# Performance work log

Hardware: AMD Instinct MI355X
Metric: run time of the kernel (lower is better)

The kernel has to match this reference:

```python
import jax, jax.numpy as jnp
import numpy as np

C = 19          # EEG channels
NP = C * C      # 361 channel pairs
D = 256         # UNIFIED_FEATURE_DIM
H = 8           # num_heads
HD = D // H     # head dim


def _build_mask():
    # rel[p, q] = True iff key-pair q shares a channel with query-pair p
    idx = np.arange(NP)
    ci, cj = idx // C, idx % C
    rel = ((ci[:, None] == ci[None, :]) | (ci[:, None] == cj[None, :]) |
           (cj[:, None] == ci[None, :]) | (cj[:, None] == cj[None, :]))
    return jnp.asarray(rel.reshape(C, C, NP))  # (channel_i, j, key_pair)

MASK = _build_mask()


def setup_inputs() -> dict:
    key = jax.random.key(0)
    ks = jax.random.split(key, 6)
    s = 0.05
    return {
        "x": jax.random.normal(ks[0], (32, NP, D), jnp.float32),
        # 19 stacked nn.MultiheadAttention modules: in_proj (3D, D) = [Wq; Wk; Wv]
        "w_in": jax.random.normal(ks[1], (C, 3 * D, D), jnp.float32) * s,
        "b_in": jnp.zeros((C, 3 * D), jnp.float32),
        "w_out": jax.random.normal(ks[2], (C, D, D), jnp.float32) * s,
        "b_out": jnp.zeros((C, D), jnp.float32),
        # fusion: nn.Linear(D, D)
        "w_fuse": jax.random.normal(ks[3], (D, D), jnp.float32) * s,
        "b_fuse": jnp.zeros((D,), jnp.float32),
    }


def reference(x, w_in, b_in, w_out, b_out, w_fuse, b_fuse):
    # x: (B, 361, D). Pair p=(i,j) at index i*19+j uses attention module i,
    # query = x[:, p], keys/values = pairs sharing channel i or j (mask).
    B = x.shape[0]
    wq, wk, wv = w_in[:, :D], w_in[:, D:2 * D], w_in[:, 2 * D:]
    bq, bk, bv = b_in[:, :D], b_in[:, D:2 * D], b_in[:, 2 * D:]

    # Per-channel K/V projections over all 361 pairs: (C, B, NP, D)
    K = jnp.einsum('bnd,ced->cbne', x, wk) + bk[:, None, None, :]
    V = jnp.einsum('bnd,ced->cbne', x, wv) + bv[:, None, None, :]
    # Queries grouped by first channel i: x reshaped to (B, C, C, D)
    xq = x.reshape(B, C, C, D)
    Q = jnp.einsum('bcjd,ced->cbje', xq, wq) + bq[:, None, None, :]  # (C,B,C,D)

    Qh = Q.reshape(C, B, C, H, HD)
    Kh = K.reshape(C, B, NP, H, HD)
    Vh = V.reshape(C, B, NP, H, HD)

    scale = 1.0 / jnp.sqrt(jnp.asarray(HD, x.dtype))
    scores = jnp.einsum('cbqhe,cbkhe->cbhqk', Qh, Kh) * scale  # (C,B,H,C,NP)
    scores = jnp.where(MASK[:, None, None, :, :], scores, -jnp.inf)
    attn = jax.nn.softmax(scores, axis=-1)

    out = jnp.einsum('cbhqk,cbkhe->cbqhe', attn, Vh).reshape(C, B, C, D)
    out = jnp.einsum('cbqd,ced->cbqe', out, w_out) + b_out[:, None, None, :]
    out = out.transpose(1, 0, 2, 3).reshape(B, NP, D)  # back to (B, 361, D)

    # fusion ('linear') + residual
    return out @ w_fuse.T + b_fuse + x
```

## Files before the change

### kernel.cpp

```cpp
#include <hip/hip_runtime.h>

#define CC 19
#define NPOS 361
#define NPAD 384
#define DIM 256
#define TKEY 32
#define NTILES 12

#define LDS_BYTES 33792

using bf16x8 = __attribute__((ext_vector_type(8))) short;
using f16x4  = __attribute__((ext_vector_type(4))) _Float16;
using floatx4 = __attribute__((ext_vector_type(4))) float;
using uintx2 = __attribute__((ext_vector_type(2))) unsigned int;

__device__ __forceinline__ unsigned short f2bf(float f) {
  unsigned u = __builtin_bit_cast(unsigned, f);
  u += 0x7fffu + ((u >> 16) & 1u);
  return (unsigned short)(u >> 16);
}

__device__ __forceinline__ f16x4 pack4h(float a, float b, float c2, float d) {
  const auto h01 = __builtin_amdgcn_cvt_pkrtz(a, b);
  const auto h23 = __builtin_amdgcn_cvt_pkrtz(c2, d);
  uintx2 uv = {__builtin_bit_cast(unsigned, h01), __builtin_bit_cast(unsigned, h23)};
  return __builtin_bit_cast(f16x4, uv);
}

__global__ void conv_all_kernel(const float* __restrict__ x,
                                const float* __restrict__ w_in,
                                const float* __restrict__ w_out,
                                const float* __restrict__ w_fuse,
                                unsigned short* __restrict__ ws) {
  const int j = blockIdx.x * 256 + threadIdx.x;
  float4 v = make_float4(0.f, 0.f, 0.f, 0.f);
  unsigned short* dst;
  if (j < 786432) {
    const int row = j >> 6;
    const int off = (j & 63) << 2;
    const int b = row / NPAD;
    const int r = row - b * NPAD;
    if (r < NPOS) v = *(const float4*)&x[(b * NPOS + r) * DIM + off];
    dst = &ws[row * DIM + off];
  } else if (j < 1720320) {
    const int k = j - 786432;
    v = *(const float4*)&w_in[k << 2];
    dst = &ws[3145728 + (k << 2)];
  } else if (j < 2031616) {
    const int k = j - 1720320;
    v = *(const float4*)&w_out[k << 2];
    dst = &ws[6881280 + (k << 2)];
  } else {
    const int k = j - 2031616;
    v = *(const float4*)&w_fuse[k << 2];
    dst = &ws[8126464 + (k << 2)];
  }
  ushort4 o;
  o.x = f2bf(v.x); o.y = f2bf(v.y); o.z = f2bf(v.z); o.w = f2bf(v.w);
  *(ushort4*)dst = o;
}

__launch_bounds__(512, 2)
__global__ void cgca_kernel(const float* __restrict__ xf,
                            const float* __restrict__ b_in,
                            const float* __restrict__ b_out,
                            const float* __restrict__ b_fuse,
                            const unsigned short* __restrict__ xbf,
                            const unsigned short* __restrict__ wibf,
                            const unsigned short* __restrict__ wobf,
                            const unsigned short* __restrict__ wfbf,
                            float* __restrict__ out) {
  const int bid = blockIdx.x;
  const int xcd = bid & 7;
  const int slot = bid >> 3;
  int c, b;
  if (slot < 64) {
    c = ((slot >> 5) << 3) + xcd;
    b = slot & 31;
  } else {
    const int widx = ((slot - 64) << 3) + xcd;
    c = 16 + (widx >> 5);
    b = widx & 31;
  }

  const int tid = threadIdx.x;
  const int w = tid >> 6;
  const int lane = tid & 63;
  const int quad = lane >> 4;
  const int l16 = lane & 15;
  const int eh = w * 32;

  extern __shared__ char smem[];
  unsigned short* bufx0 = (unsigned short*)(smem);
  unsigned short* bufx1 = (unsigned short*)(smem + 16896);
  float* sL = (float*)(smem + 16896);

  const float scale = 0.17677669529663687f;
  const floatx4 fzero = {0.f, 0.f, 0.f, 0.f};

  f16x4 qf[2][2];
  {
    bf16x8 wq[2][8];
#pragma unroll
    for (int m4 = 0; m4 < 2; ++m4)
#pragma unroll
      for (int k = 0; k < 8; ++k)
        wq[m4][k] = *(const bf16x8*)&wibf[(c * 768 + eh + m4 * 16 + l16) * DIM + k * 32 + quad * 8];
    float bq[2][4];
#pragma unroll
    for (int m4 = 0; m4 < 2; ++m4) {
      const float4 bv4 = *(const float4*)&b_in[c * 768 + eh + m4 * 16 + quad * 4];
      bq[m4][0] = bv4.x; bq[m4][1] = bv4.y; bq[m4][2] = bv4.z; bq[m4][3] = bv4.w;
    }
#pragma unroll
    for (int mt = 0; mt < 2; ++mt) {
      const int xrow = b * NPAD + c * CC + mt * 16 + l16;
      bf16x8 xq[8];
#pragma unroll
      for (int k = 0; k < 8; ++k)
        xq[k] = *(const bf16x8*)&xbf[xrow * DIM + k * 32 + quad * 8];
#pragma unroll
      for (int m4 = 0; m4 < 2; ++m4) {
        floatx4 acc = fzero;
#pragma unroll
        for (int k = 0; k < 8; ++k)
          acc = __builtin_amdgcn_mfma_f32_16x16x32_bf16(wq[m4][k], xq[k], acc, 0, 0, 0);
        qf[mt][m4] = pack4h((acc[0] + bq[m4][0]) * scale, (acc[1] + bq[m4][1]) * scale,
                            (acc[2] + bq[m4][2]) * scale, (acc[3] + bq[m4][3]) * scale);
      }
    }
  }

  bf16x8 wk[2][8], wv[2][8];
#pragma unroll
  for (int m4 = 0; m4 < 2; ++m4)
#pragma unroll
    for (int k = 0; k < 8; ++k) {
      wk[m4][k] =
          *(const bf16x8*)&wibf[(c * 768 + 256 + eh + m4 * 16 + l16) * DIM + k * 32 + quad * 8];
      wv[m4][k] =
          *(const bf16x8*)&wibf[(c * 768 + 512 + eh + m4 * 16 + l16) * DIM + k * 32 + quad * 8];
    }
  float bk[2][4];
#pragma unroll
  for (int m4 = 0; m4 < 2; ++m4) {
    const float4 bv4 = *(const float4*)&b_in[c * 768 + 256 + eh + m4 * 16 + quad * 4];
    bk[m4][0] = bv4.x; bk[m4][1] = bv4.y; bk[m4][2] = bv4.z; bk[m4][3] = bv4.w;
  }
  float bV[2];
#pragma unroll
  for (int ne = 0; ne < 2; ++ne) bV[ne] = b_in[c * 768 + 512 + eh + ne * 16 + l16];

#pragma unroll
  for (int it = 0; it < 2; ++it) {
    const int cc2 = tid + it * 512;
    const int row = cc2 >> 5;
    const int col = (cc2 & 31) * 8;
    *(bf16x8*)&bufx0[row * 264 + col] = *(const bf16x8*)&xbf[(b * NPAD + row) * DIM + col];
  }

  floatx4 o_acc[2][2];
  float lsum[2] = {0.f, 0.f};
#pragma unroll
  for (int mt = 0; mt < 2; ++mt)
#pragma unroll
    for (int ne = 0; ne < 2; ++ne) o_acc[mt][ne] = fzero;

  __syncthreads();

  for (int t = 0; t < NTILES; ++t) {
    const int t0 = t * TKEY;
    unsigned short* bx  = (t & 1) ? bufx1 : bufx0;
    unsigned short* bxn = (t & 1) ? bufx0 : bufx1;

    if (t + 1 < NTILES) {
#pragma unroll
      for (int it = 0; it < 2; ++it) {
        const int cc2 = tid + it * 512;
        const int row = cc2 >> 5;
        const int col = (cc2 & 31) * 8;
        *(bf16x8*)&bxn[row * 264 + col] =
            *(const bf16x8*)&xbf[(b * NPAD + t0 + TKEY + row) * DIM + col];
      }
    }

    floatx4 aK[2][2], aV[2][2];
#pragma unroll
    for (int i = 0; i < 2; ++i)
#pragma unroll
      for (int j = 0; j < 2; ++j) { aK[i][j] = fzero; aV[i][j] = fzero; }
#pragma unroll
    for (int k = 0; k < 8; ++k) {
      bf16x8 xfr[2];
#pragma unroll
      for (int n4 = 0; n4 < 2; ++n4)
        xfr[n4] = *(const bf16x8*)&bx[(n4 * 16 + l16) * 264 + k * 32 + quad * 8];
#pragma unroll
      for (int m4 = 0; m4 < 2; ++m4)
#pragma unroll
        for (int n4 = 0; n4 < 2; ++n4) {
          aK[m4][n4] = __builtin_amdgcn_mfma_f32_16x16x32_bf16(wk[m4][k], xfr[n4], aK[m4][n4], 0, 0, 0);
          aV[n4][m4] = __builtin_amdgcn_mfma_f32_16x16x32_bf16(xfr[n4], wv[m4][k], aV[n4][m4], 0, 0, 0);
        }
    }
    __syncthreads();

    f16x4 kf[2][2];
    f16x4 vf[2][2];
#pragma unroll
    for (int kt = 0; kt < 2; ++kt)
#pragma unroll
      for (int ec = 0; ec < 2; ++ec) {
        kf[kt][ec] = pack4h(aK[ec][kt][0] + bk[ec][0], aK[ec][kt][1] + bk[ec][1],
                            aK[ec][kt][2] + bk[ec][2], aK[ec][kt][3] + bk[ec][3]);
        vf[kt][ec] = pack4h(aV[kt][ec][0] + bV[ec], aV[kt][ec][1] + bV[ec],
                            aV[kt][ec][2] + bV[ec], aV[kt][ec][3] + bV[ec]);
      }

#pragma unroll
    for (int mt = 0; mt < 2; ++mt) {
      const unsigned q = (unsigned)(mt * 16 + l16);
      f16x4 pf[2];
#pragma unroll
      for (int kt = 0; kt < 2; ++kt) {
        floatx4 s = __builtin_amdgcn_mfma_f32_16x16x16f16(kf[kt][0], qf[mt][0], fzero, 0, 0, 0);
        s = __builtin_amdgcn_mfma_f32_16x16x16f16(kf[kt][1], qf[mt][1], s, 0, 0, 0);
        const int kbase = t0 + kt * 16 + quad * 4;
        float p[4];
#pragma unroll
        for (int r = 0; r < 4; ++r) {
          const int kabs = kbase + r;
          const unsigned ki = ((unsigned)kabs * 110377u) >> 21;
          const unsigned kj = (unsigned)kabs - ki * 19u;
          const bool ok = (kabs < NPOS) &&
                          (ki == (unsigned)c || kj == (unsigned)c || ki == q || kj == q);
          p[r] = ok ? __expf(s[r]) : 0.f;
        }
        lsum[mt] += (p[0] + p[1]) + (p[2] + p[3]);
        pf[kt] = pack4h(p[0], p[1], p[2], p[3]);
      }
#pragma unroll
      for (int kt = 0; kt < 2; ++kt)
#pragma unroll
        for (int ne = 0; ne < 2; ++ne)
          o_acc[mt][ne] =
              __builtin_amdgcn_mfma_f32_16x16x16f16(pf[kt], vf[kt][ne], o_acc[mt][ne], 0, 0, 0);
    }
  }

#pragma unroll
  for (int mt = 0; mt < 2; ++mt) {
    lsum[mt] += __shfl_xor(lsum[mt], 16);
    lsum[mt] += __shfl_xor(lsum[mt], 32);
  }
  if (lane < 16) {
    sL[w * 32 + lane] = lsum[0];
    sL[w * 32 + 16 + lane] = lsum[1];
  }
  float invl[2][4];
#pragma unroll
  for (int mt = 0; mt < 2; ++mt)
#pragma unroll
    for (int r = 0; r < 4; ++r)
      invl[mt][r] = 1.f / sL[w * 32 + mt * 16 + quad * 4 + r];

#pragma unroll
  for (int mt = 0; mt < 2; ++mt)
#pragma unroll
    for (int ne = 0; ne < 2; ++ne)
#pragma unroll
      for (int r = 0; r < 4; ++r)
        bufx0[(mt * 16 + quad * 4 + r) * 264 + eh + ne * 16 + l16] =
            f2bf(o_acc[mt][ne][r] * invl[mt][r]);
  __syncthreads();

#pragma unroll
  for (int mt = 0; mt < 2; ++mt) {
    bf16x8 a8[8];
#pragma unroll
    for (int k = 0; k < 8; ++k)
      a8[k] = *(const bf16x8*)&bufx0[(mt * 16 + l16) * 264 + k * 32 + quad * 8];
#pragma unroll
    for (int nt2 = 0; nt2 < 2; ++nt2) {
      const int e0 = w * 32 + nt2 * 16;
      floatx4 acc = fzero;
#pragma unroll
      for (int k = 0; k < 8; ++k) {
        bf16x8 b8 = *(const bf16x8*)&wobf[(c * 256 + e0 + l16) * DIM + k * 32 + quad * 8];
        acc = __builtin_amdgcn_mfma_f32_16x16x32_bf16(a8[k], b8, acc, 0, 0, 0);
      }
      const float bias = b_out[c * 256 + e0 + l16];
#pragma unroll
      for (int r = 0; r < 4; ++r)
        bufx1[(mt * 16 + quad * 4 + r) * 264 + e0 + l16] = f2bf(acc[r] + bias);
    }
  }
  __syncthreads();

#pragma unroll
  for (int mt = 0; mt < 2; ++mt) {
    bf16x8 a8[8];
#pragma unroll
    for (int k = 0; k < 8; ++k)
      a8[k] = *(const bf16x8*)&bufx1[(mt * 16 + l16) * 264 + k * 32 + quad * 8];
#pragma unroll
    for (int nt2 = 0; nt2 < 2; ++nt2) {
      const int e0 = w * 32 + nt2 * 16;
      floatx4 acc = fzero;
#pragma unroll
      for (int k = 0; k < 8; ++k) {
        bf16x8 b8 = *(const bf16x8*)&wfbf[(e0 + l16) * DIM + k * 32 + quad * 8];
        acc = __builtin_amdgcn_mfma_f32_16x16x32_bf16(a8[k], b8, acc, 0, 0, 0);
      }
      const float bfu = b_fuse[e0 + l16];
#pragma unroll
      for (int r = 0; r < 4; ++r) {
        const int row = mt * 16 + quad * 4 + r;
        if (row < CC) {
          const int gp = (b * NPOS + c * CC + row) * DIM + e0 + l16;
          out[gp] = acc[r] + bfu + xf[gp];
        }
      }
    }
  }
}

extern "C" void kernel_launch(void* const* d_in, const int* in_sizes, int n_in,
                              void* d_out, int out_size, void* d_ws, size_t ws_size,
                              hipStream_t stream) {
  const float* x      = (const float*)d_in[0];
  const float* w_in   = (const float*)d_in[1];
  const float* b_in   = (const float*)d_in[2];
  const float* w_out  = (const float*)d_in[3];
  const float* b_out  = (const float*)d_in[4];
  const float* w_fuse = (const float*)d_in[5];
  const float* b_fuse = (const float*)d_in[6];
  float* out = (float*)d_out;

  if (ws_size < (size_t)16384000) return;

  unsigned short* ws = (unsigned short*)d_ws;
  unsigned short* x_bf  = ws;
  unsigned short* wi_bf = ws + 3145728;
  unsigned short* wo_bf = ws + 6881280;
  unsigned short* wf_bf = ws + 8126464;

  conv_all_kernel<<<8000, 256, 0, stream>>>(x, w_in, w_out, w_fuse, ws);

  (void)hipFuncSetAttribute((const void*)cgca_kernel,
                            hipFuncAttributeMaxDynamicSharedMemorySize, LDS_BYTES);
  cgca_kernel<<<608, 512, LDS_BYTES, stream>>>(x, b_in, b_out, b_fuse, x_bf, wi_bf,
                                               wo_bf, wf_bf, out);
}
```

Baseline: 253.6 us.

## Stream Wk/Wv weights from global per tile instead of holding in registers

Stops keeping the K and V projection weight fragments resident in registers across all key tiles. Each tile now reloads them from global/L2 inside the loop and computes K and V in separate scoped blocks, which cuts register pressure. Launch bounds go from 2 to 4 waves-per-SIMD to raise occupancy. The cost is repeated weight loads every tile (12x more weight traffic through the cache), and there is a risk of memory stalls or spills under the tighter register budget.

```diff
diff --git a/kernel.cpp b/kernel.cpp
--- a/kernel.cpp
+++ b/kernel.cpp
@@ -60,7 +60,7 @@
   *(ushort4*)dst = o;
 }
 
-__launch_bounds__(512, 2)
+__launch_bounds__(512, 4)
 __global__ void cgca_kernel(const float* __restrict__ xf,
                             const float* __restrict__ b_in,
                             const float* __restrict__ b_out,
@@ -98,58 +98,37 @@
   const float scale = 0.17677669529663687f;
   const floatx4 fzero = {0.f, 0.f, 0.f, 0.f};
 
+  float bq[2][4], bk[2][4], bV[2];
+#pragma unroll
+  for (int m4 = 0; m4 < 2; ++m4) {
+    const float4 q4 = *(const float4*)&b_in[c * 768 + eh + m4 * 16 + quad * 4];
+    bq[m4][0] = q4.x; bq[m4][1] = q4.y; bq[m4][2] = q4.z; bq[m4][3] = q4.w;
+    const float4 k4 = *(const float4*)&b_in[c * 768 + 256 + eh + m4 * 16 + quad * 4];
+    bk[m4][0] = k4.x; bk[m4][1] = k4.y; bk[m4][2] = k4.z; bk[m4][3] = k4.w;
+    bV[m4] = b_in[c * 768 + 512 + eh + m4 * 16 + l16];
+  }
+
   f16x4 qf[2][2];
-  {
-    bf16x8 wq[2][8];
-#pragma unroll
-    for (int m4 = 0; m4 < 2; ++m4)
-#pragma unroll
-      for (int k = 0; k < 8; ++k)
-        wq[m4][k] = *(const bf16x8*)&wibf[(c * 768 + eh + m4 * 16 + l16) * DIM + k * 32 + quad * 8];
-    float bq[2][4];
+#pragma unroll
+  for (int mt = 0; mt < 2; ++mt) {
+    const int xrow = b * NPAD + c * CC + mt * 16 + l16;
+    bf16x8 xq[8];
+#pragma unroll
+    for (int k = 0; k < 8; ++k)
+      xq[k] = *(const bf16x8*)&xbf[xrow * DIM + k * 32 + quad * 8];
 #pragma unroll
     for (int m4 = 0; m4 < 2; ++m4) {
-      const float4 bv4 = *(const float4*)&b_in[c * 768 + eh + m4 * 16 + quad * 4];
-      bq[m4][0] = bv4.x; bq[m4][1] = bv4.y; bq[m4][2] = bv4.z; bq[m4][3] = bv4.w;
-    }
-#pragma unroll
-    for (int mt = 0; mt < 2; ++mt) {
-      const int xrow = b * NPAD + c * CC + mt * 16 + l16;
-      bf16x8 xq[8];
-#pragma unroll
-      for (int k = 0; k < 8; ++k)
-        xq[k] = *(const bf16x8*)&xbf[xrow * DIM + k * 32 + quad * 8];
-#pragma unroll
-      for (int m4 = 0; m4 < 2; ++m4) {
-        floatx4 acc = fzero;
-#pragma unroll
-        for (int k = 0; k < 8; ++k)
-          acc = __builtin_amdgcn_mfma_f32_16x16x32_bf16(wq[m4][k], xq[k], acc, 0, 0, 0);
-        qf[mt][m4] = pack4h((acc[0] + bq[m4][0]) * scale, (acc[1] + bq[m4][1]) * scale,
-                            (acc[2] + bq[m4][2]) * scale, (acc[3] + bq[m4][3]) * scale);
-      }
-    }
-  }
-
-  bf16x8 wk[2][8], wv[2][8];
-#pragma unroll
-  for (int m4 = 0; m4 < 2; ++m4)
-#pragma unroll
-    for (int k = 0; k < 8; ++k) {
-      wk[m4][k] =
-          *(const bf16x8*)&wibf[(c * 768 + 256 + eh + m4 * 16 + l16) * DIM + k * 32 + quad * 8];
-      wv[m4][k] =
-          *(const bf16x8*)&wibf[(c * 768 + 512 + eh + m4 * 16 + l16) * DIM + k * 32 + quad * 8];
-    }
-  float bk[2][4];
-#pragma unroll
-  for (int m4 = 0; m4 < 2; ++m4) {
-    const float4 bv4 = *(const float4*)&b_in[c * 768 + 256 + eh + m4 * 16 + quad * 4];
-    bk[m4][0] = bv4.x; bk[m4][1] = bv4.y; bk[m4][2] = bv4.z; bk[m4][3] = bv4.w;
-  }
-  float bV[2];
-#pragma unroll
-  for (int ne = 0; ne < 2; ++ne) bV[ne] = b_in[c * 768 + 512 + eh + ne * 16 + l16];
+      const unsigned short* wqp = &wibf[(c * 768 + eh + m4 * 16 + l16) * DIM + quad * 8];
+      floatx4 acc = fzero;
+#pragma unroll
+      for (int k = 0; k < 8; ++k) {
+        const bf16x8 wq = *(const bf16x8*)(wqp + k * 32);
+        acc = __builtin_amdgcn_mfma_f32_16x16x32_bf16(wq, xq[k], acc, 0, 0, 0);
+      }
+      qf[mt][m4] = pack4h((acc[0] + bq[m4][0]) * scale, (acc[1] + bq[m4][1]) * scale,
+                          (acc[2] + bq[m4][2]) * scale, (acc[3] + bq[m4][3]) * scale);
+    }
+  }
 
 #pragma unroll
   for (int it = 0; it < 2; ++it) {
@@ -165,6 +144,9 @@
   for (int mt = 0; mt < 2; ++mt)
 #pragma unroll
     for (int ne = 0; ne < 2; ++ne) o_acc[mt][ne] = fzero;
+
+  const unsigned short* wkbase = &wibf[(c * 768 + 256 + eh + l16) * DIM + quad * 8];
+  const unsigned short* wvbase = &wibf[(c * 768 + 512 + eh + l16) * DIM + quad * 8];
 
   __syncthreads();
 
@@ -184,38 +166,66 @@
       }
     }
 
-    floatx4 aK[2][2], aV[2][2];
-#pragma unroll
-    for (int i = 0; i < 2; ++i)
-#pragma unroll
-      for (int j = 0; j < 2; ++j) { aK[i][j] = fzero; aV[i][j] = fzero; }
-#pragma unroll
-    for (int k = 0; k < 8; ++k) {
-      bf16x8 xfr[2];
-#pragma unroll
-      for (int n4 = 0; n4 < 2; ++n4)
-        xfr[n4] = *(const bf16x8*)&bx[(n4 * 16 + l16) * 264 + k * 32 + quad * 8];
-#pragma unroll
-      for (int m4 = 0; m4 < 2; ++m4)
+    f16x4 kf[2][2];
+    {
+      floatx4 aK[2][2];
+#pragma unroll
+      for (int i = 0; i < 2; ++i)
+#pragma unroll
+        for (int j = 0; j < 2; ++j) aK[i][j] = fzero;
+#pragma unroll
+      for (int k = 0; k < 8; ++k) {
+        bf16x8 xfr[2], wkf[2];
 #pragma unroll
         for (int n4 = 0; n4 < 2; ++n4) {
-          aK[m4][n4] = __builtin_amdgcn_mfma_f32_16x16x32_bf16(wk[m4][k], xfr[n4], aK[m4][n4], 0, 0, 0);
-          aV[n4][m4] = __builtin_amdgcn_mfma_f32_16x16x32_bf16(xfr[n4], wv[m4][k], aV[n4][m4], 0, 0, 0);
+          xfr[n4] = *(const bf16x8*)&bx[(n4 * 16 + l16) * 264 + k * 32 + quad * 8];
+          wkf[n4] = *(const bf16x8*)(wkbase + (n4 * 16) * DIM + k * 32);
         }
+#pragma unroll
+        for (int m4 = 0; m4 < 2; ++m4)
+#pragma unroll
+          for (int n4 = 0; n4 < 2; ++n4)
+            aK[m4][n4] =
+                __builtin_amdgcn_mfma_f32_16x16x32_bf16(wkf[m4], xfr[n4], aK[m4][n4], 0, 0, 0);
+      }
+#pragma unroll
+      for (int kt = 0; kt < 2; ++kt)
+#pragma unroll
+        for (int ec = 0; ec < 2; ++ec)
+          kf[kt][ec] = pack4h(aK[ec][kt][0] + bk[ec][0], aK[ec][kt][1] + bk[ec][1],
+                              aK[ec][kt][2] + bk[ec][2], aK[ec][kt][3] + bk[ec][3]);
+    }
+
+    f16x4 vf[2][2];
+    {
+      floatx4 aV[2][2];
+#pragma unroll
+      for (int i = 0; i < 2; ++i)
+#pragma unroll
+        for (int j = 0; j < 2; ++j) aV[i][j] = fzero;
+#pragma unroll
+      for (int k = 0; k < 8; ++k) {
+        bf16x8 xfr[2], wvf[2];
+#pragma unroll
+        for (int n4 = 0; n4 < 2; ++n4) {
+          xfr[n4] = *(const bf16x8*)&bx[(n4 * 16 + l16) * 264 + k * 32 + quad * 8];
+          wvf[n4] = *(const bf16x8*)(wvbase + (n4 * 16) * DIM + k * 32);
+        }
+#pragma unroll
+        for (int m4 = 0; m4 < 2; ++m4)
+#pragma unroll
+          for (int n4 = 0; n4 < 2; ++n4)
+            aV[n4][m4] =
+                __builtin_amdgcn_mfma_f32_16x16x32_bf16(xfr[n4], wvf[m4], aV[n4][m4], 0, 0, 0);
+      }
+#pragma unroll
+      for (int kt = 0; kt < 2; ++kt)
+#pragma unroll
+        for (int ec = 0; ec < 2; ++ec)
+          vf[kt][ec] = pack4h(aV[kt][ec][0] + bV[ec], aV[kt][ec][1] + bV[ec],
+                              aV[kt][ec][2] + bV[ec], aV[kt][ec][3] + bV[ec]);
     }
     __syncthreads();
-
-    f16x4 kf[2][2];
-    f16x4 vf[2][2];
-#pragma unroll
-    for (int kt = 0; kt < 2; ++kt)
-#pragma unroll
-      for (int ec = 0; ec < 2; ++ec) {
-        kf[kt][ec] = pack4h(aK[ec][kt][0] + bk[ec][0], aK[ec][kt][1] + bk[ec][1],
-                            aK[ec][kt][2] + bk[ec][2], aK[ec][kt][3] + bk[ec][3]);
-        vf[kt][ec] = pack4h(aV[kt][ec][0] + bV[ec], aV[kt][ec][1] + bV[ec],
-                            aV[kt][ec][2] + bV[ec], aV[kt][ec][3] + bV[ec]);
-      }
 
 #pragma unroll
     for (int mt = 0; mt < 2; ++mt) {
```

Result: slower. 456.7 us (+80.1%).
